# Performance work log

Measured on AMD Instinct MI355X. Metric: run time of the kernel, lower is better.

Reference implementation:

```python
import jax, jax.numpy as jnp
import numpy as np

D_MODEL = 256
D_CLIP = 768
NHEAD = 8
HEAD_DIM = D_MODEL // NHEAD
Q_LEN = 100
B = 32
T_LEN = 1203


def setup_inputs() -> dict:
    key = jax.random.key(0)
    ks = jax.random.split(key, 16)
    xav = lambda k, o, i: jax.random.uniform(k, (o, i), jnp.float32, -1.0, 1.0) * np.sqrt(6.0 / (o + i))
    return {
        "tgt": jax.random.normal(ks[0], (Q_LEN, B, D_MODEL), jnp.float32),
        "text_classification": jax.random.normal(ks[1], (T_LEN, D_CLIP), jnp.float32),
        "query_pos": jax.random.normal(ks[2], (Q_LEN, B, D_MODEL), jnp.float32),
        "out_of_vocab_logits": jax.random.normal(ks[3], (B, Q_LEN, T_LEN), jnp.float32),
        "Wq": xav(ks[4], D_MODEL, D_MODEL), "bq": jnp.zeros((D_MODEL,), jnp.float32),
        "Wk": xav(ks[5], D_MODEL, D_CLIP), "bk": jnp.zeros((D_MODEL,), jnp.float32),
        "Wv": xav(ks[6], D_MODEL, D_CLIP), "bv": jnp.zeros((D_MODEL,), jnp.float32),
        "Wo": xav(ks[7], D_MODEL, D_MODEL), "bo": jnp.zeros((D_MODEL,), jnp.float32),
        "ln_g": jnp.ones((D_MODEL,), jnp.float32), "ln_b": jnp.zeros((D_MODEL,), jnp.float32),
        "logit_scale": jnp.asarray(np.log(1 / 0.07), jnp.float32),
    }


def _l2norm(x, eps=1e-6):
    # F.normalize: x / max(||x||, eps)
    n = jnp.sqrt(jnp.sum(x * x, axis=-1, keepdims=True))
    return x / jnp.maximum(n, eps)


def _layernorm(x, g, b, eps=1e-5):
    mu = jnp.mean(x, axis=-1, keepdims=True)
    var = jnp.mean((x - mu) ** 2, axis=-1, keepdims=True)
    return (x - mu) * jax.lax.rsqrt(var + eps) * g + b


def reference(tgt, text_classification, query_pos, out_of_vocab_logits,
              Wq, bq, Wk, bk, Wv, bv, Wo, bo, ln_g, ln_b, logit_scale):
    qin = tgt + query_pos                       # (Q, B, d_model)
    q = qin @ Wq.T + bq                         # (Q, B, d_model)
    # text embeddings shared across batch (2D path)
    k = text_classification @ Wk.T + bk         # (T, d_model)
    v = text_classification @ Wv.T + bv         # (T, d_model)

    q = q.transpose(1, 0, 2).reshape(B, Q_LEN, NHEAD, HEAD_DIM).transpose(0, 2, 1, 3)  # (B,h,Q,hd)
    k = k.reshape(T_LEN, NHEAD, HEAD_DIM).transpose(1, 0, 2)                            # (h,T,hd)
    v = v.reshape(T_LEN, NHEAD, HEAD_DIM).transpose(1, 0, 2)                            # (h,T,hd)

    q = _l2norm(q)
    k = _l2norm(k)
    scale = jnp.minimum(jnp.exp(logit_scale), 100.0)
    in_vocab = jnp.einsum('bhqd,hkd->bhqk', q, k) * scale                                # (B,h,Q,T)

    alpha = jnp.linspace(0.0, 1.0, NHEAD, dtype=in_vocab.dtype).reshape(1, NHEAD, 1, 1)
    logits = in_vocab * (1.0 - alpha) + out_of_vocab_logits[:, None] * alpha

    attn = jax.nn.softmax(logits, axis=-1)
    out = jnp.einsum('bhqk,hkd->bhqd', attn, v)                                          # (B,h,Q,hd)
    out = out.transpose(0, 2, 1, 3).reshape(B, Q_LEN, D_MODEL).transpose(1, 0, 2)        # (Q,B,d_model)
    out = out @ Wo.T + bo

    # forward_post: residual + layernorm (dropout=0)
    return _layernorm(tgt + out, ln_g, ln_b)
```

## Files before the change

### kernel.cpp

```cpp
#include <hip/hip_runtime.h>
#include <hip/hip_bf16.h>
#include <math.h>

#define D_MODEL 256
#define D_CLIP 768
#define NHEAD 8
#define HEAD_DIM 32
#define Q_LEN 100
#define BB 32
#define T_LEN 1203
#define TPAD 1216
#define MQ (Q_LEN*BB)
#define LOG2E 1.4426950408889634f

typedef __bf16 bf16_t;
typedef __bf16 bf16x8 __attribute__((ext_vector_type(8)));
typedef __bf16 bf16x4 __attribute__((ext_vector_type(4)));
typedef float f32x4 __attribute__((ext_vector_type(4)));

static __device__ __forceinline__ bf16_t to_bf16(float x) { return (bf16_t)x; }

__global__ void prep_kernel(const float* __restrict__ tgt, const float* __restrict__ qpos,
                            const float* __restrict__ text, const float* __restrict__ Wq,
                            const float* __restrict__ Wk, const float* __restrict__ Wv,
                            const float* __restrict__ Wo,
                            bf16_t* __restrict__ qin_bf, bf16_t* __restrict__ conv_dst) {
    int idx = blockIdx.x * 256 + threadIdx.x;
    if (idx >= 566848) return;
    float4 v;
    bf16_t* dst;
    if (idx < 204800) {
        float4 a = ((const float4*)tgt)[idx];
        float4 b = ((const float4*)qpos)[idx];
        v = make_float4(a.x + b.x, a.y + b.y, a.z + b.z, a.w + b.w);
        dst = qin_bf + idx * 4;
    } else {
        int j = idx - 204800;
        const float4* src;
        if (j < 230976)      src = (const float4*)text + j;
        else if (j < 247360) src = (const float4*)Wq + (j - 230976);
        else if (j < 296512) src = (const float4*)Wk + (j - 247360);
        else if (j < 345664) src = (const float4*)Wv + (j - 296512);
        else                 src = (const float4*)Wo + (j - 345664);
        v = *src;
        dst = conv_dst + (size_t)j * 4;
    }
    bf16x4 r = { to_bf16(v.x), to_bf16(v.y), to_bf16(v.z), to_bf16(v.w) };
    *(bf16x4*)dst = r;
}

__launch_bounds__(256)
__global__ void proj_kernel(const bf16_t* __restrict__ qin_bf, const bf16_t* __restrict__ text_bf,
                            const bf16_t* __restrict__ wq, const bf16_t* __restrict__ wk,
                            const bf16_t* __restrict__ wv,
                            const float* __restrict__ bq, const float* __restrict__ bk,
                            const float* __restrict__ bv,
                            bf16_t* __restrict__ qn, bf16_t* __restrict__ kn,
                            bf16_t* __restrict__ vT) {
    const int bid = blockIdx.y;
    int z, xt;
    if (bid < 50)      { z = 0; xt = bid; }
    else if (bid < 69) { z = 1; xt = bid - 50; }
    else               { z = 2; xt = bid - 69; }
    const int j = blockIdx.x;
    const int nbase = j * 32;
    const int M = (z == 0) ? MQ : T_LEN;
    const int K = (z == 0) ? D_MODEL : D_CLIP;
    const bf16_t* W = (z == 0) ? wq : (z == 1 ? wk : wv);
    const float* bias = (z == 0) ? bq : (z == 1 ? bk : bv);

    const int wave = threadIdx.x >> 6;
    const int lane = threadIdx.x & 63;
    const int c16 = lane & 15;
    const int quad = lane >> 4;
    const int mbase = xt * 64 + wave * 16;

    f32x4 a0 = (f32x4){0.f, 0.f, 0.f, 0.f};
    f32x4 a1 = (f32x4){0.f, 0.f, 0.f, 0.f};

    const int arow = (mbase + c16 < M) ? (mbase + c16) : (M - 1);
    const bf16_t* Apb = ((z == 0) ? qin_bf : text_bf) + (size_t)arow * K + quad * 8;
    const bf16_t* W0 = W + (size_t)(nbase + c16) * K + quad * 8;
    const bf16_t* W1 = W + (size_t)(nbase + 16 + c16) * K + quad * 8;
    const int ksteps = K / 32;
    #pragma unroll 4
    for (int ks = 0; ks < ksteps; ks++) {
        bf16x8 af = *(const bf16x8*)(Apb + ks * 32);
        bf16x8 b0 = *(const bf16x8*)(W0 + ks * 32);
        bf16x8 b1 = *(const bf16x8*)(W1 + ks * 32);
        a0 = __builtin_amdgcn_mfma_f32_16x16x32_bf16(af, b0, a0, 0, 0, 0);
        a1 = __builtin_amdgcn_mfma_f32_16x16x32_bf16(af, b1, a1, 0, 0, 0);
    }

    float b0s = bias[nbase + c16];
    float b1s = bias[nbase + 16 + c16];
    #pragma unroll
    for (int r = 0; r < 4; r++) { a0[r] += b0s; a1[r] += b1s; }
    if (z < 2) {
        #pragma unroll
        for (int r = 0; r < 4; r++) {
            float s = a0[r] * a0[r] + a1[r] * a1[r];
            #pragma unroll
            for (int o = 1; o < 16; o <<= 1) s += __shfl_xor(s, o);
            float sc = 1.0f / fmaxf(sqrtf(s), 1e-6f);
            a0[r] *= sc; a1[r] *= sc;
        }
    }
    #pragma unroll
    for (int r = 0; r < 4; r++) {
        int m = mbase + quad * 4 + r;
        if (m >= M) continue;
        if (z == 0) {
            int q = m >> 5, b = m & 31;
            size_t base = ((size_t)(b * NHEAD + j) * Q_LEN + q) * HEAD_DIM;
            qn[base + c16] = to_bf16(a0[r]);
            qn[base + 16 + c16] = to_bf16(a1[r]);
        } else if (z == 1) {
            size_t base = ((size_t)j * T_LEN + m) * HEAD_DIM;
            kn[base + c16] = to_bf16(a0[r]);
            kn[base + 16 + c16] = to_bf16(a1[r]);
        } else {
            vT[(size_t)(j * 32 + c16) * TPAD + m] = to_bf16(a0[r]);
            vT[(size_t)(j * 32 + 16 + c16) * TPAD + m] = to_bf16(a1[r]);
        }
    }
}

__launch_bounds__(896)
__global__ void attn_kernel(const bf16_t* __restrict__ qn, const bf16_t* __restrict__ kn,
                            const bf16_t* __restrict__ vT, const float* __restrict__ oov,
                            const float* __restrict__ logit_scale,
                            bf16_t* __restrict__ attn_out) {
    const int b = blockIdx.x;
    const int h = blockIdx.y;
    const int tid = threadIdx.x;
    const int w = tid >> 6;
    const int lane = tid & 63;
    const int c16 = lane & 15;
    const int quad = lane >> 4;
    const int qt = w >> 1;
    const int thalf = w & 1;
    const int qbase = qt * 16;

    __shared__ __align__(16) unsigned int k_lds[24320];
    __shared__ __align__(16) bf16_t p_lds[14][2][16][40];

    const float scl = fminf(expf(logit_scale[0]), 100.0f);
    const float alpha = (float)h * (1.0f / 7.0f);
    const float sscale = scl * (1.0f - alpha) * LOG2E;
    const float oscale = alpha * LOG2E;
    const float mfix = sscale + 20.0f * oscale;

    const bf16_t* knh = kn + (size_t)h * T_LEN * HEAD_DIM;
    const bf16_t* vTh = vT + (size_t)h * HEAD_DIM * TPAD;

    const int qc = (qbase + c16 < Q_LEN) ? (qbase + c16) : (Q_LEN - 1);
    bf16x8 qf = *(const bf16x8*)(qn + ((size_t)(b * NHEAD + h) * Q_LEN + qc) * HEAD_DIM + quad * 8);
    const float* oovr = oov + ((size_t)b * Q_LEN + qc) * T_LEN;
    const f32x4 zero = (f32x4){0.f, 0.f, 0.f, 0.f};

    {
        const unsigned int* knw = (const unsigned int*)knh;
        for (int idx = tid; idx < 19248; idx += 896)
            k_lds[(idx >> 4) * 20 + (idx & 15)] = knw[idx];
    }

    f32x4 olo = (f32x4){0.f, 0.f, 0.f, 0.f};
    f32x4 ohi = (f32x4){0.f, 0.f, 0.f, 0.f};
    float l_s = 0.0f;

    #define KFRAG(trow) (*(const bf16x8*)&k_lds[(unsigned)(trow) * 20 + quad * 4])
    #define LOADPV(P, vA0_, vA1_, vB0_, vB1_, oA0_, oA1_, oB0_, oB1_)                   \
        { const int tb0_ = (P) * 64; const int tb1_ = tb0_ + 32;                         \
          vA0_ = *(const bf16x8*)(vTh + (size_t)c16 * TPAD + tb0_ + quad * 8);           \
          vA1_ = *(const bf16x8*)(vTh + (size_t)(16 + c16) * TPAD + tb0_ + quad * 8);    \
          vB0_ = *(const bf16x8*)(vTh + (size_t)c16 * TPAD + tb1_ + quad * 8);           \
          vB1_ = *(const bf16x8*)(vTh + (size_t)(16 + c16) * TPAD + tb1_ + quad * 8);    \
          oA0_ = *(const float4*)(oovr + tb0_ + quad * 4);                               \
          oA1_ = *(const float4*)(oovr + tb0_ + 16 + quad * 4);                          \
          oB0_ = *(const float4*)(oovr + tb1_ + quad * 4);                               \
          oB1_ = *(const float4*)(oovr + tb1_ + 16 + quad * 4); }

    bf16x8 vA0, vA1, vB0, vB1;
    float4 oA0, oA1, oB0, oB1;
    LOADPV(thalf, vA0, vA1, vB0, vB1, oA0, oA1, oB0, oB1);

    __syncthreads();

    for (int p = thalf; p < 18; p += 2) {
        const int pn = (p + 2 < 18) ? (p + 2) : p;
        bf16x8 nvA0, nvA1, nvB0, nvB1;
        float4 noA0, noA1, noB0, noB1;
        LOADPV(pn, nvA0, nvA1, nvB0, nvB1, noA0, noA1, noB0, noB1);

        const int tb0 = p * 64, tb1 = tb0 + 32;
        f32x4 s00 = __builtin_amdgcn_mfma_f32_16x16x32_bf16(KFRAG(tb0 + c16), qf, zero, 0, 0, 0);
        f32x4 s01 = __builtin_amdgcn_mfma_f32_16x16x32_bf16(KFRAG(tb0 + 16 + c16), qf, zero, 0, 0, 0);
        f32x4 s10 = __builtin_amdgcn_mfma_f32_16x16x32_bf16(KFRAG(tb1 + c16), qf, zero, 0, 0, 0);
        f32x4 s11 = __builtin_amdgcn_mfma_f32_16x16x32_bf16(KFRAG(tb1 + 16 + c16), qf, zero, 0, 0, 0);

        float pa0[4], pa1[4], pb0[4], pb1[4];
        float ovA0[4] = {oA0.x, oA0.y, oA0.z, oA0.w};
        float ovA1[4] = {oA1.x, oA1.y, oA1.z, oA1.w};
        float ovB0[4] = {oB0.x, oB0.y, oB0.z, oB0.w};
        float ovB1[4] = {oB1.x, oB1.y, oB1.z, oB1.w};
        #pragma unroll
        for (int r = 0; r < 4; r++) {
            pa0[r] = exp2f(fmaf(s00[r], sscale, fmaf(ovA0[r], oscale, -mfix)));
            pa1[r] = exp2f(fmaf(s01[r], sscale, fmaf(ovA1[r], oscale, -mfix)));
            pb0[r] = exp2f(fmaf(s10[r], sscale, fmaf(ovB0[r], oscale, -mfix)));
            pb1[r] = exp2f(fmaf(s11[r], sscale, fmaf(ovB1[r], oscale, -mfix)));
        }
        l_s += ((pa0[0] + pa0[1]) + (pa0[2] + pa0[3])) + ((pa1[0] + pa1[1]) + (pa1[2] + pa1[3]))
             + ((pb0[0] + pb0[1]) + (pb0[2] + pb0[3])) + ((pb1[0] + pb1[1]) + (pb1[2] + pb1[3]));
        bf16x4 wA0 = { to_bf16(pa0[0]), to_bf16(pa0[1]), to_bf16(pa0[2]), to_bf16(pa0[3]) };
        bf16x4 wA1 = { to_bf16(pa1[0]), to_bf16(pa1[1]), to_bf16(pa1[2]), to_bf16(pa1[3]) };
        bf16x4 wB0 = { to_bf16(pb0[0]), to_bf16(pb0[1]), to_bf16(pb0[2]), to_bf16(pb0[3]) };
        bf16x4 wB1 = { to_bf16(pb1[0]), to_bf16(pb1[1]), to_bf16(pb1[2]), to_bf16(pb1[3]) };
        *(bf16x4*)&p_lds[w][0][c16][quad * 4] = wA0;
        *(bf16x4*)&p_lds[w][0][c16][16 + quad * 4] = wA1;
        *(bf16x4*)&p_lds[w][1][c16][quad * 4] = wB0;
        *(bf16x4*)&p_lds[w][1][c16][16 + quad * 4] = wB1;
        bf16x8 pf0 = *(const bf16x8*)(&p_lds[w][0][c16][quad * 8]);
        bf16x8 pf1 = *(const bf16x8*)(&p_lds[w][1][c16][quad * 8]);
        olo = __builtin_amdgcn_mfma_f32_16x16x32_bf16(vA0, pf0, olo, 0, 0, 0);
        ohi = __builtin_amdgcn_mfma_f32_16x16x32_bf16(vA1, pf0, ohi, 0, 0, 0);
        olo = __builtin_amdgcn_mfma_f32_16x16x32_bf16(vB0, pf1, olo, 0, 0, 0);
        ohi = __builtin_amdgcn_mfma_f32_16x16x32_bf16(vB1, pf1, ohi, 0, 0, 0);

        vA0 = nvA0; vA1 = nvA1; vB0 = nvB0; vB1 = nvB1;
        oA0 = noA0; oA1 = noA1; oB0 = noB0; oB1 = noB1;
    }

    if (thalf == 0) {
        {
            const int tb = 1152;
            f32x4 s0 = __builtin_amdgcn_mfma_f32_16x16x32_bf16(KFRAG(tb + c16), qf, zero, 0, 0, 0);
            f32x4 s1 = __builtin_amdgcn_mfma_f32_16x16x32_bf16(KFRAG(tb + 16 + c16), qf, zero, 0, 0, 0);
            float4 oa = *(const float4*)(oovr + tb + quad * 4);
            float4 oc = *(const float4*)(oovr + tb + 16 + quad * 4);
            bf16x8 v0 = *(const bf16x8*)(vTh + (size_t)c16 * TPAD + tb + quad * 8);
            bf16x8 v1 = *(const bf16x8*)(vTh + (size_t)(16 + c16) * TPAD + tb + quad * 8);
            float ova[4] = {oa.x, oa.y, oa.z, oa.w};
            float ovc[4] = {oc.x, oc.y, oc.z, oc.w};
            float p0[4], p1[4];
            #pragma unroll
            for (int r = 0; r < 4; r++) {
                p0[r] = exp2f(fmaf(s0[r], sscale, fmaf(ova[r], oscale, -mfix)));
                p1[r] = exp2f(fmaf(s1[r], sscale, fmaf(ovc[r], oscale, -mfix)));
            }
            l_s += ((p0[0] + p0[1]) + (p0[2] + p0[3])) + ((p1[0] + p1[1]) + (p1[2] + p1[3]));
            bf16x4 w0 = { to_bf16(p0[0]), to_bf16(p0[1]), to_bf16(p0[2]), to_bf16(p0[3]) };
            bf16x4 w1 = { to_bf16(p1[0]), to_bf16(p1[1]), to_bf16(p1[2]), to_bf16(p1[3]) };
            *(bf16x4*)&p_lds[w][0][c16][quad * 4] = w0;
            *(bf16x4*)&p_lds[w][0][c16][16 + quad * 4] = w1;
            bf16x8 pf = *(const bf16x8*)(&p_lds[w][0][c16][quad * 8]);
            olo = __builtin_amdgcn_mfma_f32_16x16x32_bf16(v0, pf, olo, 0, 0, 0);
            ohi = __builtin_amdgcn_mfma_f32_16x16x32_bf16(v1, pf, ohi, 0, 0, 0);
        }
        {
            const int tb = 1184;
            int tr1 = tb + 16 + c16;
            if (tr1 > T_LEN - 1) tr1 = T_LEN - 1;
            f32x4 s0 = __builtin_amdgcn_mfma_f32_16x16x32_bf16(KFRAG(tb + c16), qf, zero, 0, 0, 0);
            f32x4 s1 = __builtin_amdgcn_mfma_f32_16x16x32_bf16(KFRAG(tr1), qf, zero, 0, 0, 0);
            float4 oa = *(const float4*)(oovr + tb + quad * 4);
            bf16x8 v0 = *(const bf16x8*)(vTh + (size_t)c16 * TPAD + tb + quad * 8);
            bf16x8 v1 = *(const bf16x8*)(vTh + (size_t)(16 + c16) * TPAD + tb + quad * 8);
            float ova[4] = {oa.x, oa.y, oa.z, oa.w};
            float p0[4], p1[4];
            #pragma unroll
            for (int r = 0; r < 4; r++) {
                p0[r] = exp2f(fmaf(s0[r], sscale, fmaf(ova[r], oscale, -mfix)));
                int t2 = tb + 16 + quad * 4 + r;
                if (t2 < T_LEN) {
                    float ovc = oovr[t2];
                    p1[r] = exp2f(fmaf(s1[r], sscale, fmaf(ovc, oscale, -mfix)));
                } else {
                    p1[r] = 0.0f;
                }
            }
            l_s += ((p0[0] + p0[1]) + (p0[2] + p0[3])) + ((p1[0] + p1[1]) + (p1[2] + p1[3]));
            bf16x4 w0 = { to_bf16(p0[0]), to_bf16(p0[1]), to_bf16(p0[2]), to_bf16(p0[3]) };
            bf16x4 w1 = { to_bf16(p1[0]), to_bf16(p1[1]), to_bf16(p1[2]), to_bf16(p1[3]) };
            *(bf16x4*)&p_lds[w][1][c16][quad * 4] = w0;
            *(bf16x4*)&p_lds[w][1][c16][16 + quad * 4] = w1;
            bf16x8 pf = *(const bf16x8*)(&p_lds[w][1][c16][quad * 8]);
            olo = __builtin_amdgcn_mfma_f32_16x16x32_bf16(v0, pf, olo, 0, 0, 0);
            ohi = __builtin_amdgcn_mfma_f32_16x16x32_bf16(v1, pf, ohi, 0, 0, 0);
        }
    }
    #undef KFRAG
    #undef LOADPV

    l_s += __shfl_xor(l_s, 16);
    l_s += __shfl_xor(l_s, 32);

    __syncthreads();
    float* mrg = (float*)k_lds;
    const int mb = (thalf * 7 + qt) * 528;
    if (quad == 0) mrg[mb + c16] = l_s;
    #pragma unroll
    for (int r = 0; r < 4; r++) {
        mrg[mb + 16 + (quad * 4 + r) * 16 + c16] = olo[r];
        mrg[mb + 16 + (16 + quad * 4 + r) * 16 + c16] = ohi[r];
    }
    __syncthreads();
    if (thalf == 0) {
        const int d = lane & 31;
        const int qg = lane >> 5;
        const int b0 = qt * 528, b1 = (7 + qt) * 528;
        #pragma unroll
        for (int jj = 0; jj < 8; jj++) {
            int q16 = qg * 8 + jj;
            int qo = qbase + q16;
            if (qo < Q_LEN) {
                float L = mrg[b0 + q16] + mrg[b1 + q16];
                float O = mrg[b0 + 16 + d * 16 + q16] + mrg[b1 + 16 + d * 16 + q16];
                attn_out[((size_t)qo * BB + b) * D_MODEL + h * HEAD_DIM + d] = to_bf16(O / L);
            }
        }
    }
}

__launch_bounds__(256)
__global__ void out_kernel(const bf16_t* __restrict__ attn, const bf16_t* __restrict__ wo,
                           const float* __restrict__ bo, const float* __restrict__ tgt,
                           const float* __restrict__ ln_g, const float* __restrict__ ln_b,
                           float* __restrict__ out) {
    const int xt = blockIdx.x;
    const int wave = threadIdx.x >> 6;
    const int lane = threadIdx.x & 63;
    const int c16 = lane & 15;
    const int quad = lane >> 4;
    const int mbase = xt * 16;

    __shared__ float xs[16][264];

    f32x4 acc[4];
    #pragma unroll
    for (int i = 0; i < 4; i++) acc[i] = (f32x4){0.f, 0.f, 0.f, 0.f};
    const bf16_t* Ap = attn + (size_t)(mbase + c16) * D_MODEL + quad * 8;
    #pragma unroll
    for (int ks = 0; ks < 8; ks++) {
        bf16x8 af = *(const bf16x8*)(Ap + ks * 32);
        #pragma unroll
        for (int nt = 0; nt < 4; nt++) {
            int n = wave * 64 + nt * 16 + c16;
            bf16x8 bfr = *(const bf16x8*)(wo + (size_t)n * D_MODEL + ks * 32 + quad * 8);
            acc[nt] = __builtin_amdgcn_mfma_f32_16x16x32_bf16(af, bfr, acc[nt], 0, 0, 0);
        }
    }
    #pragma unroll
    for (int nt = 0; nt < 4; nt++) {
        int col = wave * 64 + nt * 16 + c16;
        float bb_ = bo[col];
        #pragma unroll
        for (int r = 0; r < 4; r++) {
            int m = mbase + quad * 4 + r;
            xs[quad * 4 + r][col] = acc[nt][r] + bb_ + tgt[(size_t)m * D_MODEL + col];
        }
    }
    __syncthreads();
    const int row = threadIdx.x >> 4;
    const int seg = threadIdx.x & 15;
    float sx = 0.f, sxx = 0.f;
    #pragma unroll
    for (int i = 0; i < 16; i++) {
        float x = xs[row][seg * 16 + i];
        sx += x; sxx += x * x;
    }
    #pragma unroll
    for (int o = 1; o < 16; o <<= 1) { sx += __shfl_xor(sx, o); sxx += __shfl_xor(sxx, o); }
    float mu = sx * (1.0f / 256.0f);
    float var = sxx * (1.0f / 256.0f) - mu * mu;
    float rstd = rsqrtf(fmaxf(var, 0.0f) + 1e-5f);
    size_t obase = (size_t)(mbase + row) * D_MODEL;
    #pragma unroll
    for (int i = 0; i < 16; i++) {
        int cidx = seg * 16 + i;
        out[obase + cidx] = (xs[row][cidx] - mu) * rstd * ln_g[cidx] + ln_b[cidx];
    }
}

extern "C" void kernel_launch(void* const* d_in, const int* in_sizes, int n_in,
                              void* d_out, int out_size, void* d_ws, size_t ws_size,
                              hipStream_t stream) {
    const float* tgt  = (const float*)d_in[0];
    const float* text = (const float*)d_in[1];
    const float* qpos = (const float*)d_in[2];
    const float* oov  = (const float*)d_in[3];
    const float* Wq = (const float*)d_in[4];
    const float* bq = (const float*)d_in[5];
    const float* Wk = (const float*)d_in[6];
    const float* bk = (const float*)d_in[7];
    const float* Wv = (const float*)d_in[8];
    const float* bv = (const float*)d_in[9];
    const float* Wo = (const float*)d_in[10];
    const float* bo = (const float*)d_in[11];
    const float* ln_g = (const float*)d_in[12];
    const float* ln_b = (const float*)d_in[13];
    const float* lsc  = (const float*)d_in[14];

    bf16_t* wsb = (bf16_t*)d_ws;
    bf16_t* text_bf = wsb + 0;
    bf16_t* wq_bf   = wsb + 923904;
    bf16_t* wk_bf   = wsb + 989440;
    bf16_t* wv_bf   = wsb + 1186048;
    bf16_t* wo_bf   = wsb + 1382656;
    bf16_t* qin_bf  = wsb + 1448192;
    bf16_t* qn      = wsb + 2267392;
    bf16_t* kn      = wsb + 3086592;
    bf16_t* vT      = wsb + 3394560;
    bf16_t* attn    = wsb + 3705856;
    float* out      = (float*)d_out;

    prep_kernel<<<2215, 256, 0, stream>>>(tgt, qpos, text, Wq, Wk, Wv, Wo, qin_bf, text_bf);
    proj_kernel<<<dim3(8, 88, 1), 256, 0, stream>>>(qin_bf, text_bf, wq_bf, wk_bf, wv_bf,
                                                    bq, bk, bv, qn, kn, vT);
    attn_kernel<<<dim3(32, 8), 896, 0, stream>>>(qn, kn, vT, oov, lsc, attn);
    out_kernel<<<200, 256, 0, stream>>>(attn, wo_bf, bo, tgt, ln_g, ln_b, out);
}
```

Measured before the change: 158.6 us.

## Fuse four kernels into one cooperative persistent kernel with grid syncs

Replaces the prep, projection, attention and output kernels with a single cooperative kernel of 256 blocks by 896 threads, separated by grid-wide syncs. The aim is to remove three kernel launch gaps and their tail effects. In exchange, the projection and output phases now run on a fixed grid, with many threads idle in the output phase. Each grid sync adds its own cost, and the large LDS and thread count per block limit occupancy.

```diff
diff --git a/kernel.cpp b/kernel.cpp
--- a/kernel.cpp
+++ b/kernel.cpp
@@ -1,6 +1,9 @@
 #include <hip/hip_runtime.h>
 #include <hip/hip_bf16.h>
+#include <hip/hip_cooperative_groups.h>
 #include <math.h>
+
+namespace cg = cooperative_groups;
 
 #define D_MODEL 256
 #define D_CLIP 768
@@ -20,366 +23,368 @@
 
 static __device__ __forceinline__ bf16_t to_bf16(float x) { return (bf16_t)x; }
 
-__global__ void prep_kernel(const float* __restrict__ tgt, const float* __restrict__ qpos,
-                            const float* __restrict__ text, const float* __restrict__ Wq,
-                            const float* __restrict__ Wk, const float* __restrict__ Wv,
-                            const float* __restrict__ Wo,
-                            bf16_t* __restrict__ qin_bf, bf16_t* __restrict__ conv_dst) {
-    int idx = blockIdx.x * 256 + threadIdx.x;
-    if (idx >= 566848) return;
-    float4 v;
-    bf16_t* dst;
-    if (idx < 204800) {
-        float4 a = ((const float4*)tgt)[idx];
-        float4 b = ((const float4*)qpos)[idx];
-        v = make_float4(a.x + b.x, a.y + b.y, a.z + b.z, a.w + b.w);
-        dst = qin_bf + idx * 4;
-    } else {
-        int j = idx - 204800;
-        const float4* src;
-        if (j < 230976)      src = (const float4*)text + j;
-        else if (j < 247360) src = (const float4*)Wq + (j - 230976);
-        else if (j < 296512) src = (const float4*)Wk + (j - 247360);
-        else if (j < 345664) src = (const float4*)Wv + (j - 296512);
-        else                 src = (const float4*)Wo + (j - 345664);
-        v = *src;
-        dst = conv_dst + (size_t)j * 4;
-    }
-    bf16x4 r = { to_bf16(v.x), to_bf16(v.y), to_bf16(v.z), to_bf16(v.w) };
-    *(bf16x4*)dst = r;
-}
-
-__launch_bounds__(256)
-__global__ void proj_kernel(const bf16_t* __restrict__ qin_bf, const bf16_t* __restrict__ text_bf,
-                            const bf16_t* __restrict__ wq, const bf16_t* __restrict__ wk,
-                            const bf16_t* __restrict__ wv,
-                            const float* __restrict__ bq, const float* __restrict__ bk,
-                            const float* __restrict__ bv,
-                            bf16_t* __restrict__ qn, bf16_t* __restrict__ kn,
-                            bf16_t* __restrict__ vT) {
-    const int bid = blockIdx.y;
-    int z, xt;
-    if (bid < 50)      { z = 0; xt = bid; }
-    else if (bid < 69) { z = 1; xt = bid - 50; }
-    else               { z = 2; xt = bid - 69; }
-    const int j = blockIdx.x;
-    const int nbase = j * 32;
-    const int M = (z == 0) ? MQ : T_LEN;
-    const int K = (z == 0) ? D_MODEL : D_CLIP;
-    const bf16_t* W = (z == 0) ? wq : (z == 1 ? wk : wv);
-    const float* bias = (z == 0) ? bq : (z == 1 ? bk : bv);
-
-    const int wave = threadIdx.x >> 6;
-    const int lane = threadIdx.x & 63;
-    const int c16 = lane & 15;
-    const int quad = lane >> 4;
-    const int mbase = xt * 64 + wave * 16;
-
-    f32x4 a0 = (f32x4){0.f, 0.f, 0.f, 0.f};
-    f32x4 a1 = (f32x4){0.f, 0.f, 0.f, 0.f};
-
-    const int arow = (mbase + c16 < M) ? (mbase + c16) : (M - 1);
-    const bf16_t* Apb = ((z == 0) ? qin_bf : text_bf) + (size_t)arow * K + quad * 8;
-    const bf16_t* W0 = W + (size_t)(nbase + c16) * K + quad * 8;
-    const bf16_t* W1 = W + (size_t)(nbase + 16 + c16) * K + quad * 8;
-    const int ksteps = K / 32;
-    #pragma unroll 4
-    for (int ks = 0; ks < ksteps; ks++) {
-        bf16x8 af = *(const bf16x8*)(Apb + ks * 32);
-        bf16x8 b0 = *(const bf16x8*)(W0 + ks * 32);
-        bf16x8 b1 = *(const bf16x8*)(W1 + ks * 32);
-        a0 = __builtin_amdgcn_mfma_f32_16x16x32_bf16(af, b0, a0, 0, 0, 0);
-        a1 = __builtin_amdgcn_mfma_f32_16x16x32_bf16(af, b1, a1, 0, 0, 0);
-    }
-
-    float b0s = bias[nbase + c16];
-    float b1s = bias[nbase + 16 + c16];
-    #pragma unroll
-    for (int r = 0; r < 4; r++) { a0[r] += b0s; a1[r] += b1s; }
-    if (z < 2) {
-        #pragma unroll
-        for (int r = 0; r < 4; r++) {
-            float s = a0[r] * a0[r] + a1[r] * a1[r];
-            #pragma unroll
-            for (int o = 1; o < 16; o <<= 1) s += __shfl_xor(s, o);
-            float sc = 1.0f / fmaxf(sqrtf(s), 1e-6f);
-            a0[r] *= sc; a1[r] *= sc;
-        }
-    }
-    #pragma unroll
-    for (int r = 0; r < 4; r++) {
-        int m = mbase + quad * 4 + r;
-        if (m >= M) continue;
-        if (z == 0) {
-            int q = m >> 5, b = m & 31;
-            size_t base = ((size_t)(b * NHEAD + j) * Q_LEN + q) * HEAD_DIM;
-            qn[base + c16] = to_bf16(a0[r]);
-            qn[base + 16 + c16] = to_bf16(a1[r]);
-        } else if (z == 1) {
-            size_t base = ((size_t)j * T_LEN + m) * HEAD_DIM;
-            kn[base + c16] = to_bf16(a0[r]);
-            kn[base + 16 + c16] = to_bf16(a1[r]);
-        } else {
-            vT[(size_t)(j * 32 + c16) * TPAD + m] = to_bf16(a0[r]);
-            vT[(size_t)(j * 32 + 16 + c16) * TPAD + m] = to_bf16(a1[r]);
-        }
-    }
-}
-
 __launch_bounds__(896)
-__global__ void attn_kernel(const bf16_t* __restrict__ qn, const bf16_t* __restrict__ kn,
-                            const bf16_t* __restrict__ vT, const float* __restrict__ oov,
-                            const float* __restrict__ logit_scale,
-                            bf16_t* __restrict__ attn_out) {
-    const int b = blockIdx.x;
-    const int h = blockIdx.y;
+__global__ void fused_kernel(const float* __restrict__ tgt, const float* __restrict__ qpos,
+                             const float* __restrict__ text,
+                             const float* __restrict__ Wq, const float* __restrict__ Wk,
+                             const float* __restrict__ Wv, const float* __restrict__ Wo,
+                             const float* __restrict__ oov,
+                             const float* __restrict__ bq, const float* __restrict__ bk,
+                             const float* __restrict__ bv, const float* __restrict__ bo,
+                             const float* __restrict__ ln_g, const float* __restrict__ ln_b,
+                             const float* __restrict__ lsc,
+                             bf16_t* __restrict__ ws, float* __restrict__ out) {
+    cg::grid_group grid = cg::this_grid();
+
+    __shared__ __align__(16) unsigned int k_lds[24320];
+    __shared__ __align__(16) bf16_t p_lds[14][2][16][40];
+
+    bf16_t* text_bf = ws;
+    bf16_t* wq_bf   = ws + 923904;
+    bf16_t* wk_bf   = ws + 989440;
+    bf16_t* wv_bf   = ws + 1186048;
+    bf16_t* wo_bf   = ws + 1382656;
+    bf16_t* qin_bf  = ws + 1448192;
+    bf16_t* qn      = ws + 2267392;
+    bf16_t* kn      = ws + 3086592;
+    bf16_t* vT      = ws + 3394560;
+    bf16_t* attn_ws = ws + 3705856;
+
     const int tid = threadIdx.x;
-    const int w = tid >> 6;
+    const int blk = blockIdx.x;
     const int lane = tid & 63;
     const int c16 = lane & 15;
     const int quad = lane >> 4;
-    const int qt = w >> 1;
-    const int thalf = w & 1;
-    const int qbase = qt * 16;
-
-    __shared__ __align__(16) unsigned int k_lds[24320];
-    __shared__ __align__(16) bf16_t p_lds[14][2][16][40];
-
-    const float scl = fminf(expf(logit_scale[0]), 100.0f);
-    const float alpha = (float)h * (1.0f / 7.0f);
-    const float sscale = scl * (1.0f - alpha) * LOG2E;
-    const float oscale = alpha * LOG2E;
-    const float mfix = sscale + 20.0f * oscale;
-
-    const bf16_t* knh = kn + (size_t)h * T_LEN * HEAD_DIM;
-    const bf16_t* vTh = vT + (size_t)h * HEAD_DIM * TPAD;
-
-    const int qc = (qbase + c16 < Q_LEN) ? (qbase + c16) : (Q_LEN - 1);
-    bf16x8 qf = *(const bf16x8*)(qn + ((size_t)(b * NHEAD + h) * Q_LEN + qc) * HEAD_DIM + quad * 8);
-    const float* oovr = oov + ((size_t)b * Q_LEN + qc) * T_LEN;
-    const f32x4 zero = (f32x4){0.f, 0.f, 0.f, 0.f};
+
+    for (int idx = blk * 896 + tid; idx < 566848; idx += 229376) {
+        if (idx < 204800) {
+            float4 a = ((const float4*)tgt)[idx];
+            float4 b = ((const float4*)qpos)[idx];
+            bf16x4 r = { to_bf16(a.x + b.x), to_bf16(a.y + b.y),
+                         to_bf16(a.z + b.z), to_bf16(a.w + b.w) };
+            *(bf16x4*)(qin_bf + (size_t)idx * 4) = r;
+        } else {
+            int j = idx - 204800;
+            const float4* src;
+            if (j < 230976)      src = (const float4*)text + j;
+            else if (j < 247360) src = (const float4*)Wq + (j - 230976);
+            else if (j < 296512) src = (const float4*)Wk + (j - 247360);
+            else if (j < 345664) src = (const float4*)Wv + (j - 296512);
+            else                 src = (const float4*)Wo + (j - 345664);
+            float4 v = *src;
+            bf16x4 r = { to_bf16(v.x), to_bf16(v.y), to_bf16(v.z), to_bf16(v.w) };
+            *(bf16x4*)(text_bf + (size_t)j * 4) = r;
+        }
+    }
+    grid.sync();
 
     {
-        const unsigned int* knw = (const unsigned int*)knh;
-        for (int idx = tid; idx < 19248; idx += 896)
-            k_lds[(idx >> 4) * 20 + (idx & 15)] = knw[idx];
+        const int gw = blk * 14 + (tid >> 6);
+        if (gw < 2816) {
+            const int wv4 = gw & 3;
+            const int j = (gw >> 2) & 7;
+            const int bid = gw >> 5;
+            int z, xt;
+            if (bid < 50)      { z = 0; xt = bid; }
+            else if (bid < 69) { z = 1; xt = bid - 50; }
+            else               { z = 2; xt = bid - 69; }
+            const int nbase = j * 32;
+            const int M = (z == 0) ? MQ : T_LEN;
+            const int K = (z == 0) ? D_MODEL : D_CLIP;
+            const bf16_t* W = (z == 0) ? wq_bf : (z == 1 ? wk_bf : wv_bf);
+            const float* bias = (z == 0) ? bq : (z == 1 ? bk : bv);
+            const int mbase = xt * 64 + wv4 * 16;
+
+            f32x4 a0 = (f32x4){0.f, 0.f, 0.f, 0.f};
+            f32x4 a1 = (f32x4){0.f, 0.f, 0.f, 0.f};
+            const int arow = (mbase + c16 < M) ? (mbase + c16) : (M - 1);
+            const bf16_t* Apb = ((z == 0) ? qin_bf : text_bf) + (size_t)arow * K + quad * 8;
+            const bf16_t* W0 = W + (size_t)(nbase + c16) * K + quad * 8;
+            const bf16_t* W1 = W + (size_t)(nbase + 16 + c16) * K + quad * 8;
+            const int ksteps = K / 32;
+            #pragma unroll 4
+            for (int ks = 0; ks < ksteps; ks++) {
+                bf16x8 af = *(const bf16x8*)(Apb + ks * 32);
+                bf16x8 b0 = *(const bf16x8*)(W0 + ks * 32);
+                bf16x8 b1 = *(const bf16x8*)(W1 + ks * 32);
+                a0 = __builtin_amdgcn_mfma_f32_16x16x32_bf16(af, b0, a0, 0, 0, 0);
+                a1 = __builtin_amdgcn_mfma_f32_16x16x32_bf16(af, b1, a1, 0, 0, 0);
+            }
+            float b0s = bias[nbase + c16];
+            float b1s = bias[nbase + 16 + c16];
+            #pragma unroll
+            for (int r = 0; r < 4; r++) { a0[r] += b0s; a1[r] += b1s; }
+            if (z < 2) {
+                #pragma unroll
+                for (int r = 0; r < 4; r++) {
+                    float s = a0[r] * a0[r] + a1[r] * a1[r];
+                    #pragma unroll
+                    for (int o = 1; o < 16; o <<= 1) s += __shfl_xor(s, o);
+                    float sc = 1.0f / fmaxf(sqrtf(s), 1e-6f);
+                    a0[r] *= sc; a1[r] *= sc;
+                }
+            }
+            #pragma unroll
+            for (int r = 0; r < 4; r++) {
+                int m = mbase + quad * 4 + r;
+                if (m >= M) continue;
+                if (z == 0) {
+                    int q = m >> 5, b = m & 31;
+                    size_t base = ((size_t)(b * NHEAD + j) * Q_LEN + q) * HEAD_DIM;
+                    qn[base + c16] = to_bf16(a0[r]);
+                    qn[base + 16 + c16] = to_bf16(a1[r]);
+                } else if (z == 1) {
+                    size_t base = ((size_t)j * T_LEN + m) * HEAD_DIM;
+                    kn[base + c16] = to_bf16(a0[r]);
+                    kn[base + 16 + c16] = to_bf16(a1[r]);
+                } else {
+                    vT[(size_t)(j * 32 + c16) * TPAD + m] = to_bf16(a0[r]);
+                    vT[(size_t)(j * 32 + 16 + c16) * TPAD + m] = to_bf16(a1[r]);
+                }
+            }
+        }
     }
-
-    f32x4 olo = (f32x4){0.f, 0.f, 0.f, 0.f};
-    f32x4 ohi = (f32x4){0.f, 0.f, 0.f, 0.f};
-    float l_s = 0.0f;
-
-    #define KFRAG(trow) (*(const bf16x8*)&k_lds[(unsigned)(trow) * 20 + quad * 4])
-    #define LOADPV(P, vA0_, vA1_, vB0_, vB1_, oA0_, oA1_, oB0_, oB1_)                   \
-        { const int tb0_ = (P) * 64; const int tb1_ = tb0_ + 32;                         \
-          vA0_ = *(const bf16x8*)(vTh + (size_t)c16 * TPAD + tb0_ + quad * 8);           \
-          vA1_ = *(const bf16x8*)(vTh + (size_t)(16 + c16) * TPAD + tb0_ + quad * 8);    \
-          vB0_ = *(const bf16x8*)(vTh + (size_t)c16 * TPAD + tb1_ + quad * 8);           \
-          vB1_ = *(const bf16x8*)(vTh + (size_t)(16 + c16) * TPAD + tb1_ + quad * 8);    \
-          oA0_ = *(const float4*)(oovr + tb0_ + quad * 4);                               \
-          oA1_ = *(const float4*)(oovr + tb0_ + 16 + quad * 4);                          \
-          oB0_ = *(const float4*)(oovr + tb1_ + quad * 4);                               \
-          oB1_ = *(const float4*)(oovr + tb1_ + 16 + quad * 4); }
-
-    bf16x8 vA0, vA1, vB0, vB1;
-    float4 oA0, oA1, oB0, oB1;
-    LOADPV(thalf, vA0, vA1, vB0, vB1, oA0, oA1, oB0, oB1);
-
-    __syncthreads();
-
-    for (int p = thalf; p < 18; p += 2) {
-        const int pn = (p + 2 < 18) ? (p + 2) : p;
-        bf16x8 nvA0, nvA1, nvB0, nvB1;
-        float4 noA0, noA1, noB0, noB1;
-        LOADPV(pn, nvA0, nvA1, nvB0, nvB1, noA0, noA1, noB0, noB1);
-
-        const int tb0 = p * 64, tb1 = tb0 + 32;
-        f32x4 s00 = __builtin_amdgcn_mfma_f32_16x16x32_bf16(KFRAG(tb0 + c16), qf, zero, 0, 0, 0);
-        f32x4 s01 = __builtin_amdgcn_mfma_f32_16x16x32_bf16(KFRAG(tb0 + 16 + c16), qf, zero, 0, 0, 0);
-        f32x4 s10 = __builtin_amdgcn_mfma_f32_16x16x32_bf16(KFRAG(tb1 + c16), qf, zero, 0, 0, 0);
-        f32x4 s11 = __builtin_amdgcn_mfma_f32_16x16x32_bf16(KFRAG(tb1 + 16 + c16), qf, zero, 0, 0, 0);
-
-        float pa0[4], pa1[4], pb0[4], pb1[4];
-        float ovA0[4] = {oA0.x, oA0.y, oA0.z, oA0.w};
-        float ovA1[4] = {oA1.x, oA1.y, oA1.z, oA1.w};
-        float ovB0[4] = {oB0.x, oB0.y, oB0.z, oB0.w};
-        float ovB1[4] = {oB1.x, oB1.y, oB1.z, oB1.w};
+    grid.sync();
+
+    {
+        const int b = blk & 31;
+        const int h = blk >> 5;
+        const int w = tid >> 6;
+        const int qt = w >> 1;
+        const int thalf = w & 1;
+        const int qbase = qt * 16;
+
+        const float scl = fminf(expf(lsc[0]), 100.0f);
+        const float alpha = (float)h * (1.0f / 7.0f);
+        const float sscale = scl * (1.0f - alpha) * LOG2E;
+        const float oscale = alpha * LOG2E;
+        const float mfix = sscale + 20.0f * oscale;
+
+        const bf16_t* knh = kn + (size_t)h * T_LEN * HEAD_DIM;
+        const bf16_t* vTh = vT + (size_t)h * HEAD_DIM * TPAD;
+
+        const int qc = (qbase + c16 < Q_LEN) ? (qbase + c16) : (Q_LEN - 1);
+        bf16x8 qf = *(const bf16x8*)(qn + ((size_t)(b * NHEAD + h) * Q_LEN + qc) * HEAD_DIM + quad * 8);
+        const float* oovr = oov + ((size_t)b * Q_LEN + qc) * T_LEN;
+        const f32x4 zero = (f32x4){0.f, 0.f, 0.f, 0.f};
+
+        {
+            const unsigned int* knw = (const unsigned int*)knh;
+            for (int idx = tid; idx < 19248; idx += 896)
+                k_lds[(idx >> 4) * 20 + (idx & 15)] = knw[idx];
+        }
+
+        f32x4 olo = (f32x4){0.f, 0.f, 0.f, 0.f};
+        f32x4 ohi = (f32x4){0.f, 0.f, 0.f, 0.f};
+        float l_s = 0.0f;
+
+        #define KFRAG(trow) (*(const bf16x8*)&k_lds[(unsigned)(trow) * 20 + quad * 4])
+        #define LOADPV(P, vA0_, vA1_, vB0_, vB1_, oA0_, oA1_, oB0_, oB1_)                   \
+            { const int tb0_ = (P) * 64; const int tb1_ = tb0_ + 32;                         \
+              vA0_ = *(const bf16x8*)(vTh + (size_t)c16 * TPAD + tb0_ + quad * 8);           \
+              vA1_ = *(const bf16x8*)(vTh + (size_t)(16 + c16) * TPAD + tb0_ + quad * 8);    \
+              vB0_ = *(const bf16x8*)(vTh + (size_t)c16 * TPAD + tb1_ + quad * 8);           \
+              vB1_ = *(const bf16x8*)(vTh + (size_t)(16 + c16) * TPAD + tb1_ + quad * 8);    \
+              oA0_ = *(const float4*)(oovr + tb0_ + quad * 4);                               \
+              oA1_ = *(const float4*)(oovr + tb0_ + 16 + quad * 4);                          \
+              oB0_ = *(const float4*)(oovr + tb1_ + quad * 4);                               \
+              oB1_ = *(const float4*)(oovr + tb1_ + 16 + quad * 4); }
+
+        bf16x8 vA0, vA1, vB0, vB1;
+        float4 oA0, oA1, oB0, oB1;
+        LOADPV(thalf, vA0, vA1, vB0, vB1, oA0, oA1, oB0, oB1);
+
+        __syncthreads();
+
+        for (int p = thalf; p < 18; p += 2) {
+            const int pn = (p + 2 < 18) ? (p + 2) : p;
+            bf16x8 nvA0, nvA1, nvB0, nvB1;
+            float4 noA0, noA1, noB0, noB1;
+            LOADPV(pn, nvA0, nvA1, nvB0, nvB1, noA0, noA1, noB0, noB1);
+
+            const int tb0 = p * 64, tb1 = tb0 + 32;
+            f32x4 s00 = __builtin_amdgcn_mfma_f32_16x16x32_bf16(KFRAG(tb0 + c16), qf, zero, 0, 0, 0);
+            f32x4 s01 = __builtin_amdgcn_mfma_f32_16x16x32_bf16(KFRAG(tb0 + 16 + c16), qf, zero, 0, 0, 0);
+            f32x4 s10 = __builtin_amdgcn_mfma_f32_16x16x32_bf16(KFRAG(tb1 + c16), qf, zero, 0, 0, 0);
+            f32x4 s11 = __builtin_amdgcn_mfma_f32_16x16x32_bf16(KFRAG(tb1 + 16 + c16), qf, zero, 0, 0, 0);
+
+            float pa0[4], pa1[4], pb0[4], pb1[4];
+            float ovA0[4] = {oA0.x, oA0.y, oA0.z, oA0.w};
+            float ovA1[4] = {oA1.x, oA1.y, oA1.z, oA1.w};
+            float ovB0[4] = {oB0.x, oB0.y, oB0.z, oB0.w};
+            float ovB1[4] = {oB1.x, oB1.y, oB1.z, oB1.w};
+            #pragma unroll
+            for (int r = 0; r < 4; r++) {
+                pa0[r] = exp2f(fmaf(s00[r], sscale, fmaf(ovA0[r], oscale, -mfix)));
+                pa1[r] = exp2f(fmaf(s01[r], sscale, fmaf(ovA1[r], oscale, -mfix)));
+                pb0[r] = exp2f(fmaf(s10[r], sscale, fmaf(ovB0[r], oscale, -mfix)));
+                pb1[r] = exp2f(fmaf(s11[r], sscale, fmaf(ovB1[r], oscale, -mfix)));
+            }
+            l_s += ((pa0[0] + pa0[1]) + (pa0[2] + pa0[3])) + ((pa1[0] + pa1[1]) + (pa1[2] + pa1[3]))
+                 + ((pb0[0] + pb0[1]) + (pb0[2] + pb0[3])) + ((pb1[0] + pb1[1]) + (pb1[2] + pb1[3]));
+            bf16x4 wA0 = { to_bf16(pa0[0]), to_bf16(pa0[1]), to_bf16(pa0[2]), to_bf16(pa0[3]) };
+            bf16x4 wA1 = { to_bf16(pa1[0]), to_bf16(pa1[1]), to_bf16(pa1[2]), to_bf16(pa1[3]) };
+            bf16x4 wB0 = { to_bf16(pb0[0]), to_bf16(pb0[1]), to_bf16(pb0[2]), to_bf16(pb0[3]) };
+            bf16x4 wB1 = { to_bf16(pb1[0]), to_bf16(pb1[1]), to_bf16(pb1[2]), to_bf16(pb1[3]) };
+            *(bf16x4*)&p_lds[w][0][c16][quad * 4] = wA0;
+            *(bf16x4*)&p_lds[w][0][c16][16 + quad * 4] = wA1;
+            *(bf16x4*)&p_lds[w][1][c16][quad * 4] = wB0;
+            *(bf16x4*)&p_lds[w][1][c16][16 + quad * 4] = wB1;
+            bf16x8 pf0 = *(const bf16x8*)(&p_lds[w][0][c16][quad * 8]);
+            bf16x8 pf1 = *(const bf16x8*)(&p_lds[w][1][c16][quad * 8]);
+            olo = __builtin_amdgcn_mfma_f32_16x16x32_bf16(vA0, pf0, olo, 0, 0, 0);
+            ohi = __builtin_amdgcn_mfma_f32_16x16x32_bf16(vA1, pf0, ohi, 0, 0, 0);
+            olo = __builtin_amdgcn_mfma_f32_16x16x32_bf16(vB0, pf1, olo, 0, 0, 0);
+            ohi = __builtin_amdgcn_mfma_f32_16x16x32_bf16(vB1, pf1, ohi, 0, 0, 0);
+
+            vA0 = nvA0; vA1 = nvA1; vB0 = nvB0; vB1 = nvB1;
+            oA0 = noA0; oA1 = noA1; oB0 = noB0; oB1 = noB1;
+        }
+
+        if (thalf == 0) {
+            {
+                const int tb = 1152;
+                f32x4 s0 = __builtin_amdgcn_mfma_f32_16x16x32_bf16(KFRAG(tb + c16), qf, zero, 0, 0, 0);
+                f32x4 s1 = __builtin_amdgcn_mfma_f32_16x16x32_bf16(KFRAG(tb + 16 + c16), qf, zero, 0, 0, 0);
+                float4 oa = *(const float4*)(oovr + tb + quad * 4);
+                float4 oc = *(const float4*)(oovr + tb + 16 + quad * 4);
+                bf16x8 v0 = *(const bf16x8*)(vTh + (size_t)c16 * TPAD + tb + quad * 8);
+                bf16x8 v1 = *(const bf16x8*)(vTh + (size_t)(16 + c16) * TPAD + tb + quad * 8);
+                float ova[4] = {oa.x, oa.y, oa.z, oa.w};
+                float ovc[4] = {oc.x, oc.y, oc.z, oc.w};
+                float p0[4], p1[4];
+                #pragma unroll
+                for (int r = 0; r < 4; r++) {
+                    p0[r] = exp2f(fmaf(s0[r], sscale, fmaf(ova[r], oscale, -mfix)));
+                    p1[r] = exp2f(fmaf(s1[r], sscale, fmaf(ovc[r], oscale, -mfix)));
+                }
+                l_s += ((p0[0] + p0[1]) + (p0[2] + p0[3])) + ((p1[0] + p1[1]) + (p1[2] + p1[3]));
+                bf16x4 w0 = { to_bf16(p0[0]), to_bf16(p0[1]), to_bf16(p0[2]), to_bf16(p0[3]) };
+                bf16x4 w1 = { to_bf16(p1[0]), to_bf16(p1[1]), to_bf16(p1[2]), to_bf16(p1[3]) };
+                *(bf16x4*)&p_lds[w][0][c16][quad * 4] = w0;
+                *(bf16x4*)&p_lds[w][0][c16][16 + quad * 4] = w1;
+                bf16x8 pf = *(const bf16x8*)(&p_lds[w][0][c16][quad * 8]);
+                olo = __builtin_amdgcn_mfma_f32_16x16x32_bf16(v0, pf, olo, 0, 0, 0);
+                ohi = __builtin_amdgcn_mfma_f32_16x16x32_bf16(v1, pf, ohi, 0, 0, 0);
+            }
+            {
+                const int tb = 1184;
+                int tr1 = tb + 16 + c16;
+                if (tr1 > T_LEN - 1) tr1 = T_LEN - 1;
+                f32x4 s0 = __builtin_amdgcn_mfma_f32_16x16x32_bf16(KFRAG(tb + c16), qf, zero, 0, 0, 0);
+                f32x4 s1 = __builtin_amdgcn_mfma_f32_16x16x32_bf16(KFRAG(tr1), qf, zero, 0, 0, 0);
+                float4 oa = *(const float4*)(oovr + tb + quad * 4);
+                bf16x8 v0 = *(const bf16x8*)(vTh + (size_t)c16 * TPAD + tb + quad * 8);
+                bf16x8 v1 = *(const bf16x8*)(vTh + (size_t)(16 + c16) * TPAD + tb + quad * 8);
+                float ova[4] = {oa.x, oa.y, oa.z, oa.w};
+                float p0[4], p1[4];
+                #pragma unroll
+                for (int r = 0; r < 4; r++) {
+                    p0[r] = exp2f(fmaf(s0[r], sscale, fmaf(ova[r], oscale, -mfix)));
+                    int t2 = tb + 16 + quad * 4 + r;
+                    if (t2 < T_LEN) {
+                        float ovc = oovr[t2];
+                        p1[r] = exp2f(fmaf(s1[r], sscale, fmaf(ovc, oscale, -mfix)));
+                    } else {
+                        p1[r] = 0.0f;
+                    }
+                }
+                l_s += ((p0[0] + p0[1]) + (p0[2] + p0[3])) + ((p1[0] + p1[1]) + (p1[2] + p1[3]));
+                bf16x4 w0 = { to_bf16(p0[0]), to_bf16(p0[1]), to_bf16(p0[2]), to_bf16(p0[3]) };
+                bf16x4 w1 = { to_bf16(p1[0]), to_bf16(p1[1]), to_bf16(p1[2]), to_bf16(p1[3]) };
+                *(bf16x4*)&p_lds[w][1][c16][quad * 4] = w0;
+                *(bf16x4*)&p_lds[w][1][c16][16 + quad * 4] = w1;
+                bf16x8 pf = *(const bf16x8*)(&p_lds[w][1][c16][quad * 8]);
+                olo = __builtin_amdgcn_mfma_f32_16x16x32_bf16(v0, pf, olo, 0, 0, 0);
+                ohi = __builtin_amdgcn_mfma_f32_16x16x32_bf16(v1, pf, ohi, 0, 0, 0);
+            }
+        }
+        #undef KFRAG
+        #undef LOADPV
+
+        l_s += __shfl_xor(l_s, 16);
+        l_s += __shfl_xor(l_s, 32);
+
+        __syncthreads();
+        float* mrg = (float*)k_lds;
+        const int mb = (thalf * 7 + qt) * 528;
+        if (quad == 0) mrg[mb + c16] = l_s;
         #pragma unroll
         for (int r = 0; r < 4; r++) {
-            pa0[r] = exp2f(fmaf(s00[r], sscale, fmaf(ovA0[r], oscale, -mfix)));
-            pa1[r] = exp2f(fmaf(s01[r], sscale, fmaf(ovA1[r], oscale, -mfix)));
-            pb0[r] = exp2f(fmaf(s10[r], sscale, fmaf(ovB0[r], oscale, -mfix)));
-            pb1[r] = exp2f(fmaf(s11[r], sscale, fmaf(ovB1[r], oscale, -mfix)));
-        }
-        l_s += ((pa0[0] + pa0[1]) + (pa0[2] + pa0[3])) + ((pa1[0] + pa1[1]) + (pa1[2] + pa1[3]))
-             + ((pb0[0] + pb0[1]) + (pb0[2] + pb0[3])) + ((pb1[0] + pb1[1]) + (pb1[2] + pb1[3]));
-        bf16x4 wA0 = { to_bf16(pa0[0]), to_bf16(pa0[1]), to_bf16(pa0[2]), to_bf16(pa0[3]) };
-        bf16x4 wA1 = { to_bf16(pa1[0]), to_bf16(pa1[1]), to_bf16(pa1[2]), to_bf16(pa1[3]) };
-        bf16x4 wB0 = { to_bf16(pb0[0]), to_bf16(pb0[1]), to_bf16(pb0[2]), to_bf16(pb0[3]) };
-        bf16x4 wB1 = { to_bf16(pb1[0]), to_bf16(pb1[1]), to_bf16(pb1[2]), to_bf16(pb1[3]) };
-        *(bf16x4*)&p_lds[w][0][c16][quad * 4] = wA0;
-        *(bf16x4*)&p_lds[w][0][c16][16 + quad * 4] = wA1;
-        *(bf16x4*)&p_lds[w][1][c16][quad * 4] = wB0;
-        *(bf16x4*)&p_lds[w][1][c16][16 + quad * 4] = wB1;
-        bf16x8 pf0 = *(const bf16x8*)(&p_lds[w][0][c16][quad * 8]);
-        bf16x8 pf1 = *(const bf16x8*)(&p_lds[w][1][c16][quad * 8]);
-        olo = __builtin_amdgcn_mfma_f32_16x16x32_bf16(vA0, pf0, olo, 0, 0, 0);
-        ohi = __builtin_amdgcn_mfma_f32_16x16x32_bf16(vA1, pf0, ohi, 0, 0, 0);
-        olo = __builtin_amdgcn_mfma_f32_16x16x32_bf16(vB0, pf1, olo, 0, 0, 0);
-        ohi = __builtin_amdgcn_mfma_f32_16x16x32_bf16(vB1, pf1, ohi, 0, 0, 0);
-
-        vA0 = nvA0; vA1 = nvA1; vB0 = nvB0; vB1 = nvB1;
-        oA0 = noA0; oA1 = noA1; oB0 = noB0; oB1 = noB1;
+            mrg[mb + 16 + (quad * 4 + r) * 16 + c16] = olo[r];
+            mrg[mb + 16 + (16 + quad * 4 + r) * 16 + c16] = ohi[r];
+        }
+        __syncthreads();
+        if (thalf == 0) {
+            const int d = lane & 31;
+            const int qg = lane >> 5;
+            const int b0 = qt * 528, b1 = (7 + qt) * 528;
+            #pragma unroll
+            for (int jj = 0; jj < 8; jj++) {
+                int q16 = qg * 8 + jj;
+                int qo = qbase + q16;
+                if (qo < Q_LEN) {
+                    float L = mrg[b0 + q16] + mrg[b1 + q16];
+                    float O = mrg[b0 + 16 + d * 16 + q16] + mrg[b1 + 16 + d * 16 + q16];
+                    attn_ws[((size_t)qo * BB + b) * D_MODEL + h * HEAD_DIM + d] = to_bf16(O / L);
+                }
+            }
+        }
     }
-
-    if (thalf == 0) {
-        {
-            const int tb = 1152;
-            f32x4 s0 = __builtin_amdgcn_mfma_f32_16x16x32_bf16(KFRAG(tb + c16), qf, zero, 0, 0, 0);
-            f32x4 s1 = __builtin_amdgcn_mfma_f32_16x16x32_bf16(KFRAG(tb + 16 + c16), qf, zero, 0, 0, 0);
-            float4 oa = *(const float4*)(oovr + tb + quad * 4);
-            float4 oc = *(const float4*)(oovr + tb + 16 + quad * 4);
-            bf16x8 v0 = *(const bf16x8*)(vTh + (size_t)c16 * TPAD + tb + quad * 8);
-            bf16x8 v1 = *(const bf16x8*)(vTh + (size_t)(16 + c16) * TPAD + tb + quad * 8);
-            float ova[4] = {oa.x, oa.y, oa.z, oa.w};
-            float ovc[4] = {oc.x, oc.y, oc.z, oc.w};
-            float p0[4], p1[4];
-            #pragma unroll
-            for (int r = 0; r < 4; r++) {
-                p0[r] = exp2f(fmaf(s0[r], sscale, fmaf(ova[r], oscale, -mfix)));
-                p1[r] = exp2f(fmaf(s1[r], sscale, fmaf(ovc[r], oscale, -mfix)));
-            }
-            l_s += ((p0[0] + p0[1]) + (p0[2] + p0[3])) + ((p1[0] + p1[1]) + (p1[2] + p1[3]));
-            bf16x4 w0 = { to_bf16(p0[0]), to_bf16(p0[1]), to_bf16(p0[2]), to_bf16(p0[3]) };
-            bf16x4 w1 = { to_bf16(p1[0]), to_bf16(p1[1]), to_bf16(p1[2]), to_bf16(p1[3]) };
-            *(bf16x4*)&p_lds[w][0][c16][quad * 4] = w0;
-            *(bf16x4*)&p_lds[w][0][c16][16 + quad * 4] = w1;
-            bf16x8 pf = *(const bf16x8*)(&p_lds[w][0][c16][quad * 8]);
-            olo = __builtin_amdgcn_mfma_f32_16x16x32_bf16(v0, pf, olo, 0, 0, 0);
-            ohi = __builtin_amdgcn_mfma_f32_16x16x32_bf16(v1, pf, ohi, 0, 0, 0);
-        }
-        {
-            const int tb = 1184;
-            int tr1 = tb + 16 + c16;
-            if (tr1 > T_LEN - 1) tr1 = T_LEN - 1;
-            f32x4 s0 = __builtin_amdgcn_mfma_f32_16x16x32_bf16(KFRAG(tb + c16), qf, zero, 0, 0, 0);
-            f32x4 s1 = __builtin_amdgcn_mfma_f32_16x16x32_bf16(KFRAG(tr1), qf, zero, 0, 0, 0);
-            float4 oa = *(const float4*)(oovr + tb + quad * 4);
-            bf16x8 v0 = *(const bf16x8*)(vTh + (size_t)c16 * TPAD + tb + quad * 8);
-            bf16x8 v1 = *(const bf16x8*)(vTh + (size_t)(16 + c16) * TPAD + tb + quad * 8);
-            float ova[4] = {oa.x, oa.y, oa.z, oa.w};
-            float p0[4], p1[4];
-            #pragma unroll
-            for (int r = 0; r < 4; r++) {
-                p0[r] = exp2f(fmaf(s0[r], sscale, fmaf(ova[r], oscale, -mfix)));
-                int t2 = tb + 16 + quad * 4 + r;
-                if (t2 < T_LEN) {
-                    float ovc = oovr[t2];
-                    p1[r] = exp2f(fmaf(s1[r], sscale, fmaf(ovc, oscale, -mfix)));
-                } else {
-                    p1[r] = 0.0f;
-                }
-            }
-            l_s += ((p0[0] + p0[1]) + (p0[2] + p0[3])) + ((p1[0] + p1[1]) + (p1[2] + p1[3]));
-            bf16x4 w0 = { to_bf16(p0[0]), to_bf16(p0[1]), to_bf16(p0[2]), to_bf16(p0[3]) };
-            bf16x4 w1 = { to_bf16(p1[0]), to_bf16(p1[1]), to_bf16(p1[2]), to_bf16(p1[3]) };
-            *(bf16x4*)&p_lds[w][1][c16][quad * 4] = w0;
-            *(bf16x4*)&p_lds[w][1][c16][16 + quad * 4] = w1;
-            bf16x8 pf = *(const bf16x8*)(&p_lds[w][1][c16][quad * 8]);
-            olo = __builtin_amdgcn_mfma_f32_16x16x32_bf16(v0, pf, olo, 0, 0, 0);
-            ohi = __builtin_amdgcn_mfma_f32_16x16x32_bf16(v1, pf, ohi, 0, 0, 0);
-        }
-    }
-    #undef KFRAG
-    #undef LOADPV
-
-    l_s += __shfl_xor(l_s, 16);
-    l_s += __shfl_xor(l_s, 32);
-
-    __syncthreads();
-    float* mrg = (float*)k_lds;
-    const int mb = (thalf * 7 + qt) * 528;
-    if (quad == 0) mrg[mb + c16] = l_s;
-    #pragma unroll
-    for (int r = 0; r < 4; r++) {
-        mrg[mb + 16 + (quad * 4 + r) * 16 + c16] = olo[r];
-        mrg[mb + 16 + (16 + quad * 4 + r) * 16 + c16] = ohi[r];
-    }
-    __syncthreads();
-    if (thalf == 0) {
-        const int d = lane & 31;
-        const int qg = lane >> 5;
-        const int b0 = qt * 528, b1 = (7 + qt) * 528;
-        #pragma unroll
-        for (int jj = 0; jj < 8; jj++) {
-            int q16 = qg * 8 + jj;
-            int qo = qbase + q16;
-            if (qo < Q_LEN) {
-                float L = mrg[b0 + q16] + mrg[b1 + q16];
-                float O = mrg[b0 + 16 + d * 16 + q16] + mrg[b1 + 16 + d * 16 + q16];
-                attn_out[((size_t)qo * BB + b) * D_MODEL + h * HEAD_DIM + d] = to_bf16(O / L);
-            }
-        }
-    }
-}
-
-__launch_bounds__(256)
-__global__ void out_kernel(const bf16_t* __restrict__ attn, const bf16_t* __restrict__ wo,
-                           const float* __restrict__ bo, const float* __restrict__ tgt,
-                           const float* __restrict__ ln_g, const float* __restrict__ ln_b,
-                           float* __restrict__ out) {
-    const int xt = blockIdx.x;
-    const int wave = threadIdx.x >> 6;
-    const int lane = threadIdx.x & 63;
-    const int c16 = lane & 15;
-    const int quad = lane >> 4;
-    const int mbase = xt * 16;
-
-    __shared__ float xs[16][264];
-
-    f32x4 acc[4];
-    #pragma unroll
-    for (int i = 0; i < 4; i++) acc[i] = (f32x4){0.f, 0.f, 0.f, 0.f};
-    const bf16_t* Ap = attn + (size_t)(mbase + c16) * D_MODEL + quad * 8;
-    #pragma unroll
-    for (int ks = 0; ks < 8; ks++) {
-        bf16x8 af = *(const bf16x8*)(Ap + ks * 32);
-        #pragma unroll
-        for (int nt = 0; nt < 4; nt++) {
-            int n = wave * 64 + nt * 16 + c16;
-            bf16x8 bfr = *(const bf16x8*)(wo + (size_t)n * D_MODEL + ks * 32 + quad * 8);
-            acc[nt] = __builtin_amdgcn_mfma_f32_16x16x32_bf16(af, bfr, acc[nt], 0, 0, 0);
-        }
-    }
-    #pragma unroll
-    for (int nt = 0; nt < 4; nt++) {
-        int col = wave * 64 + nt * 16 + c16;
-        float bb_ = bo[col];
-        #pragma unroll
-        for (int r = 0; r < 4; r++) {
-            int m = mbase + quad * 4 + r;
-            xs[quad * 4 + r][col] = acc[nt][r] + bb_ + tgt[(size_t)m * D_MODEL + col];
-        }
-    }
-    __syncthreads();
-    const int row = threadIdx.x >> 4;
-    const int seg = threadIdx.x & 15;
-    float sx = 0.f, sxx = 0.f;
-    #pragma unroll
-    for (int i = 0; i < 16; i++) {
-        float x = xs[row][seg * 16 + i];
-        sx += x; sxx += x * x;
-    }
-    #pragma unroll
-    for (int o = 1; o < 16; o <<= 1) { sx += __shfl_xor(sx, o); sxx += __shfl_xor(sxx, o); }
-    float mu = sx * (1.0f / 256.0f);
-    float var = sxx * (1.0f / 256.0f) - mu * mu;
-    float rstd = rsqrtf(fmaxf(var, 0.0f) + 1e-5f);
-    size_t obase = (size_t)(mbase + row) * D_MODEL;
-    #pragma unroll
-    for (int i = 0; i < 16; i++) {
-        int cidx = seg * 16 + i;
-        out[obase + cidx] = (xs[row][cidx] - mu) * rstd * ln_g[cidx] + ln_b[cidx];
+    grid.sync();
+
+    if (blk < 200) {
+        float (*xs)[264] = (float(*)[264])k_lds;
+        const int mbase = blk * 16;
+        if (tid < 256) {
+            const int wave = tid >> 6;
+            f32x4 acc[4];
+            #pragma unroll
+            for (int i = 0; i < 4; i++) acc[i] = (f32x4){0.f, 0.f, 0.f, 0.f};
+            const bf16_t* Ap = attn_ws + (size_t)(mbase + c16) * D_MODEL + quad * 8;
+            #pragma unroll
+            for (int ks = 0; ks < 8; ks++) {
+                bf16x8 af = *(const bf16x8*)(Ap + ks * 32);
+                #pragma unroll
+                for (int nt = 0; nt < 4; nt++) {
+                    int n = wave * 64 + nt * 16 + c16;
+                    bf16x8 bfr = *(const bf16x8*)(wo_bf + (size_t)n * D_MODEL + ks * 32 + quad * 8);
+                    acc[nt] = __builtin_amdgcn_mfma_f32_16x16x32_bf16(af, bfr, acc[nt], 0, 0, 0);
+                }
+            }
+            #pragma unroll
+            for (int nt = 0; nt < 4; nt++) {
+                int col = wave * 64 + nt * 16 + c16;
+                float bb_ = bo[col];
+                #pragma unroll
+                for (int r = 0; r < 4; r++) {
+                    int m = mbase + quad * 4 + r;
+                    xs[quad * 4 + r][col] = acc[nt][r] + bb_ + tgt[(size_t)m * D_MODEL + col];
+                }
+            }
+        }
+        __syncthreads();
+        if (tid < 256) {
+            const int row = tid >> 4;
+            const int seg = tid & 15;
+            float sx = 0.f, sxx = 0.f;
+            #pragma unroll
+            for (int i = 0; i < 16; i++) {
+                float x = xs[row][seg * 16 + i];
+                sx += x; sxx += x * x;
+            }
+            #pragma unroll
+            for (int o = 1; o < 16; o <<= 1) { sx += __shfl_xor(sx, o); sxx += __shfl_xor(sxx, o); }
+            float mu = sx * (1.0f / 256.0f);
+            float var = sxx * (1.0f / 256.0f) - mu * mu;
+            float rstd = rsqrtf(fmaxf(var, 0.0f) + 1e-5f);
+            size_t obase = (size_t)(mbase + row) * D_MODEL;
+            #pragma unroll
+            for (int i = 0; i < 16; i++) {
+                int cidx = seg * 16 + i;
+                out[obase + cidx] = (xs[row][cidx] - mu) * rstd * ln_g[cidx] + ln_b[cidx];
+            }
+        }
     }
 }
 
@@ -402,22 +407,11 @@
     const float* ln_b = (const float*)d_in[13];
     const float* lsc  = (const float*)d_in[14];
 
-    bf16_t* wsb = (bf16_t*)d_ws;
-    bf16_t* text_bf = wsb + 0;
-    bf16_t* wq_bf   = wsb + 923904;
-    bf16_t* wk_bf   = wsb + 989440;
-    bf16_t* wv_bf   = wsb + 1186048;
-    bf16_t* wo_bf   = wsb + 1382656;
-    bf16_t* qin_bf  = wsb + 1448192;
-    bf16_t* qn      = wsb + 2267392;
-    bf16_t* kn      = wsb + 3086592;
-    bf16_t* vT      = wsb + 3394560;
-    bf16_t* attn    = wsb + 3705856;
-    float* out      = (float*)d_out;
-
-    prep_kernel<<<2215, 256, 0, stream>>>(tgt, qpos, text, Wq, Wk, Wv, Wo, qin_bf, text_bf);
-    proj_kernel<<<dim3(8, 88, 1), 256, 0, stream>>>(qin_bf, text_bf, wq_bf, wk_bf, wv_bf,
-                                                    bq, bk, bv, qn, kn, vT);
-    attn_kernel<<<dim3(32, 8), 896, 0, stream>>>(qn, kn, vT, oov, lsc, attn);
-    out_kernel<<<200, 256, 0, stream>>>(attn, wo_bf, bo, tgt, ln_g, ln_b, out);
+    bf16_t* ws = (bf16_t*)d_ws;
+    float* outp = (float*)d_out;
+
+    void* args[] = { &tgt, &qpos, &text, &Wq, &Wk, &Wv, &Wo, &oov,
+                     &bq, &bk, &bv, &bo, &ln_g, &ln_b, &lsc, &ws, &outp };
+    hipLaunchCooperativeKernel((const void*)fused_kernel, dim3(256), dim3(896),
+                               args, 0, stream);
 }
```

Result: slower. 281.4 us (+77.4%).
